# Kernel optimization log

Hardware: AMD Instinct MI355X
Metric: run time of the kernel (lower is better)

Reference implementation:

```python
import jax, jax.numpy as jnp
import numpy as np

DIM = 4096
EPS = 1e-5


def setup_inputs() -> dict:
    key = jax.random.key(0)
    k_x, k_w, k_b, k_g, k_be = jax.random.split(key, 5)
    x = jax.random.normal(k_x, (4, 4096, DIM), dtype=jnp.float32)
    # Linear params (PyTorch default init scale ~ 1/sqrt(dim))
    scale = 1.0 / np.sqrt(DIM)
    W = jax.random.uniform(k_w, (DIM, DIM), dtype=jnp.float32, minval=-scale, maxval=scale)
    b = jax.random.uniform(k_b, (DIM,), dtype=jnp.float32, minval=-scale, maxval=scale)
    # LayerNorm affine params
    gamma = jnp.ones((DIM,), dtype=jnp.float32)
    beta = jnp.zeros((DIM,), dtype=jnp.float32)
    return {"x": x, "W": W, "b": b, "gamma": gamma, "beta": beta}


def reference(x, W, b, gamma, beta) -> jnp.ndarray:
    # LayerNorm over last dim (eps=1e-5, matching nn.LayerNorm default)
    mean = jnp.mean(x, axis=-1, keepdims=True)
    var = jnp.mean(jnp.square(x - mean), axis=-1, keepdims=True)
    h = (x - mean) * jax.lax.rsqrt(var + EPS) * gamma + beta
    # Linear: y = h @ W^T + b  (torch Linear stores W as [out, in])
    y = jnp.einsum("bsd,ed->bse", h, W) + b
    # ReLU
    return jnp.maximum(y, 0.0)
```

## Files before the change

kernel.cpp:

```cpp
#include <hip/hip_runtime.h>

#define DIM 4096
#define MROWS 16384
#define EPSV 1e-5f
#define NKT (DIM / 64)

typedef __attribute__((ext_vector_type(8))) short short8;
typedef __attribute__((ext_vector_type(4))) float floatx4;

__device__ __forceinline__ unsigned short f2bf(float f) {
  union { float f; unsigned u; } c; c.f = f;
  unsigned r = c.u + 0x7fffu + ((c.u >> 16) & 1u);
  return (unsigned short)(r >> 16);
}

struct alignas(16) US8 { unsigned short u[8]; };

__global__ __launch_bounds__(256) void ln_kernel(const float* __restrict__ x,
                                                 const float* __restrict__ gamma,
                                                 const float* __restrict__ beta,
                                                 unsigned short* __restrict__ h) {
  const int row  = blockIdx.x * 4 + (threadIdx.x >> 6);
  const int lane = threadIdx.x & 63;
  const float4* xr = (const float4*)(x + (size_t)row * DIM);
  float4 v[16];
  float s = 0.f, s2 = 0.f;
#pragma unroll
  for (int t = 0; t < 8; ++t) {
    const int idx = lane * 2 + t * 128;
    v[2 * t]     = xr[idx];
    v[2 * t + 1] = xr[idx + 1];
#pragma unroll
    for (int j = 0; j < 2; ++j) {
      const float4 q = v[2 * t + j];
      s  += q.x + q.y + q.z + q.w;
      s2 += q.x * q.x + q.y * q.y + q.z * q.z + q.w * q.w;
    }
  }
#pragma unroll
  for (int off = 32; off > 0; off >>= 1) {
    s  += __shfl_xor(s, off);
    s2 += __shfl_xor(s2, off);
  }
  const float mean = s * (1.f / DIM);
  const float var  = s2 * (1.f / DIM) - mean * mean;
  const float rstd = rsqrtf(var + EPSV);
  const float4* g4 = (const float4*)gamma;
  const float4* b4 = (const float4*)beta;
  US8* hr = (US8*)(h + (size_t)row * DIM);
#pragma unroll
  for (int t = 0; t < 8; ++t) {
    const int idx = lane * 2 + t * 128;
    US8 o;
#pragma unroll
    for (int j = 0; j < 2; ++j) {
      const float4 g = g4[idx + j], b = b4[idx + j], q = v[2 * t + j];
      o.u[4 * j + 0] = f2bf((q.x - mean) * rstd * g.x + b.x);
      o.u[4 * j + 1] = f2bf((q.y - mean) * rstd * g.y + b.y);
      o.u[4 * j + 2] = f2bf((q.z - mean) * rstd * g.z + b.z);
      o.u[4 * j + 3] = f2bf((q.w - mean) * rstd * g.w + b.w);
    }
    hr[lane + t * 64] = o;
  }
}

__global__ __launch_bounds__(256) void wconv(const float* __restrict__ W,
                                             unsigned short* __restrict__ Wb) {
  const int i = blockIdx.x * 256 + threadIdx.x;
  const float4 w0 = ((const float4*)W)[2 * i];
  const float4 w1 = ((const float4*)W)[2 * i + 1];
  US8 o;
  o.u[0] = f2bf(w0.x); o.u[1] = f2bf(w0.y); o.u[2] = f2bf(w0.z); o.u[3] = f2bf(w0.w);
  o.u[4] = f2bf(w1.x); o.u[5] = f2bf(w1.y); o.u[6] = f2bf(w1.z); o.u[7] = f2bf(w1.w);
  ((US8*)Wb)[i] = o;
}

template <int MH, int NH>
__device__ __forceinline__ void mma_q(floatx4 acc[8][4], const short8 a[2][4], const short8 b[2][2]) {
  __builtin_amdgcn_s_setprio(1);
#pragma unroll
  for (int ks = 0; ks < 2; ++ks)
#pragma unroll
    for (int mf = 0; mf < 4; ++mf)
#pragma unroll
      for (int nf = 0; nf < 2; ++nf)
        acc[MH * 4 + mf][NH * 2 + nf] = __builtin_amdgcn_mfma_f32_16x16x32_bf16(
            a[ks][mf], b[ks][nf], acc[MH * 4 + mf][NH * 2 + nf], 0, 0, 0);
  __builtin_amdgcn_s_setprio(0);
}

#define BAR()    __builtin_amdgcn_s_barrier()
#define LGKM0()  asm volatile("s_waitcnt lgkmcnt(0)" ::: "memory")
#define VMCNT4() asm volatile("s_waitcnt vmcnt(4)" ::: "memory")
#define VMCNT0() asm volatile("s_waitcnt vmcnt(0)" ::: "memory")

__global__ __launch_bounds__(512, 2) void gemm_bt(const unsigned short* __restrict__ A,
                                                  const unsigned short* __restrict__ B,
                                                  const float* __restrict__ bias,
                                                  float* __restrict__ out) {
  __shared__ short8 As8[4096];
  __shared__ short8 Bs8[4096];
  const int tid  = threadIdx.x;
  const int lane = tid & 63, wave = tid >> 6;
  const int warp_m = wave >> 2, warp_n = wave & 3;
  const int fr = lane & 15;
  const int cg = lane >> 4;

  const int pid = blockIdx.x;
  const int xcd = pid & 7;
  const int s   = pid >> 3;
  const int bm0 = (s >> 1) * 256;
  const int bn0 = (xcd * 2 + (s & 1)) * 256;

  auto stage = [&](const unsigned short* __restrict__ g, short8* lds, int rowbase, int k0, int h) {
#pragma unroll
    for (int i = 0; i < 2; ++i) {
      const int q = i * 512 + wave * 64 + lane;
      const int r = h * 128 + (q >> 3);
      const int c = (q & 7) ^ (r & 7);
      const unsigned short* src = g + (size_t)(rowbase + r) * DIM + k0 + c * 8;
      __builtin_amdgcn_global_load_lds((const __attribute__((address_space(1))) void*)src,
                                       (__attribute__((address_space(3))) void*)(lds + h * 1024 + i * 512 + wave * 64),
                                       16, 0, 0);
    }
  };
  auto ld_a = [&](short8 a[2][4], int buf, int rbase) {
#pragma unroll
    for (int ks = 0; ks < 2; ++ks)
#pragma unroll
      for (int mf = 0; mf < 4; ++mf) {
        const int r = rbase + mf * 16 + fr;
        a[ks][mf] = As8[buf * 2048 + r * 8 + ((ks * 4 + cg) ^ (r & 7))];
      }
  };
  auto ld_b = [&](short8 b[2][2], int buf, int rbase) {
#pragma unroll
    for (int ks = 0; ks < 2; ++ks)
#pragma unroll
      for (int nf = 0; nf < 2; ++nf) {
        const int r = rbase + nf * 16 + fr;
        b[ks][nf] = Bs8[buf * 2048 + r * 8 + ((ks * 4 + cg) ^ (r & 7))];
      }
  };

  floatx4 acc[8][4];
#pragma unroll
  for (int i = 0; i < 8; ++i)
#pragma unroll
    for (int j = 0; j < 4; ++j)
#pragma unroll
      for (int r = 0; r < 4; ++r) acc[i][j][r] = 0.f;

  const int Ra0 = warp_m * 128;
  const int Rb0 = warp_n * 64;

  stage(A, As8, bm0, 0, 0);
  stage(A, As8, bm0, 0, 1);
  stage(B, Bs8, bn0, 0, 0);
  stage(B, Bs8, bn0, 0, 1);
  stage(B, Bs8 + 2048, bn0, 64, 0);
  stage(B, Bs8 + 2048, bn0, 64, 1);
  VMCNT4();
  BAR();

  short8 a[2][4], b0[2][2], b1[2][2];

  for (int it = 0; it < NKT / 2; ++it) {
    const int kO  = it * 128 + 64;
    const int kE2 = (2 * it + 2 < NKT ? 2 * it + 2 : NKT - 1) * 64;
    const int kO2 = (2 * it + 3 < NKT ? 2 * it + 3 : NKT - 1) * 64;

    ld_a(a, 0, Ra0);
    ld_b(b0, 0, Rb0);
    stage(A, As8 + 2048, bm0, kO, 0);
    BAR(); LGKM0();
    mma_q<0, 0>(acc, a, b0);
    BAR();

    ld_b(b1, 0, Rb0 + 32);
    stage(A, As8 + 2048, bm0, kO, 1);
    BAR(); LGKM0();
    mma_q<0, 1>(acc, a, b1);
    BAR();

    ld_a(a, 0, Ra0 + 64);
    stage(B, Bs8, bn0, kE2, 0);
    BAR(); LGKM0();
    mma_q<1, 0>(acc, a, b0);
    BAR();

    stage(B, Bs8, bn0, kE2, 1);
    VMCNT4();
    BAR(); LGKM0();
    mma_q<1, 1>(acc, a, b1);
    BAR();

    ld_a(a, 1, Ra0);
    ld_b(b0, 1, Rb0);
    stage(A, As8, bm0, kE2, 0);
    BAR(); LGKM0();
    mma_q<0, 0>(acc, a, b0);
    BAR();

    ld_b(b1, 1, Rb0 + 32);
    stage(A, As8, bm0, kE2, 1);
    BAR(); LGKM0();
    mma_q<0, 1>(acc, a, b1);
    BAR();

    ld_a(a, 1, Ra0 + 64);
    stage(B, Bs8 + 2048, bn0, kO2, 0);
    BAR(); LGKM0();
    mma_q<1, 0>(acc, a, b0);
    BAR();

    stage(B, Bs8 + 2048, bn0, kO2, 1);
    VMCNT4();
    BAR(); LGKM0();
    mma_q<1, 1>(acc, a, b1);
    BAR();
  }

  VMCNT0();

#pragma unroll
  for (int nh = 0; nh < 2; ++nh)
#pragma unroll
    for (int nf = 0; nf < 2; ++nf) {
      const int col = bn0 + warp_n * 64 + nh * 32 + nf * 16 + fr;
      const float bv = bias[col];
#pragma unroll
      for (int mh = 0; mh < 2; ++mh)
#pragma unroll
        for (int mf = 0; mf < 4; ++mf) {
          const int rbase = bm0 + warp_m * 128 + mh * 64 + mf * 16 + cg * 4;
          const floatx4 v = acc[mh * 4 + mf][nh * 2 + nf];
#pragma unroll
          for (int r = 0; r < 4; ++r)
            out[(size_t)(rbase + r) * DIM + col] = fmaxf(v[r] + bv, 0.f);
        }
    }
}

__global__ __launch_bounds__(256) void fallback_kernel(const float* __restrict__ x,
                                                       const float* __restrict__ W,
                                                       const float* __restrict__ bias,
                                                       const float* __restrict__ gamma,
                                                       const float* __restrict__ beta,
                                                       float* __restrict__ out) {
  __shared__ float h[DIM];
  __shared__ float red[8];
  const int row = blockIdx.x, tid = threadIdx.x;
  const float4* xr = (const float4*)(x + (size_t)row * DIM);
  float s = 0.f, s2 = 0.f;
  float4 v[4];
#pragma unroll
  for (int i = 0; i < 4; ++i) {
    v[i] = xr[tid + i * 256];
    s  += v[i].x + v[i].y + v[i].z + v[i].w;
    s2 += v[i].x * v[i].x + v[i].y * v[i].y + v[i].z * v[i].z + v[i].w * v[i].w;
  }
#pragma unroll
  for (int off = 32; off > 0; off >>= 1) {
    s  += __shfl_down(s, off);
    s2 += __shfl_down(s2, off);
  }
  const int lane = tid & 63, wave = tid >> 6;
  if (lane == 0) { red[wave] = s; red[wave + 4] = s2; }
  __syncthreads();
  s  = red[0] + red[1] + red[2] + red[3];
  s2 = red[4] + red[5] + red[6] + red[7];
  const float mean = s * (1.f / DIM);
  const float var  = s2 * (1.f / DIM) - mean * mean;
  const float rstd = rsqrtf(var + EPSV);
#pragma unroll
  for (int i = 0; i < 4; ++i) {
    const int idx = tid + i * 256;
    const float4 g = ((const float4*)gamma)[idx];
    const float4 b = ((const float4*)beta)[idx];
    float4 o;
    o.x = (v[i].x - mean) * rstd * g.x + b.x;
    o.y = (v[i].y - mean) * rstd * g.y + b.y;
    o.z = (v[i].z - mean) * rstd * g.z + b.z;
    o.w = (v[i].w - mean) * rstd * g.w + b.w;
    ((float4*)h)[idx] = o;
  }
  __syncthreads();
  for (int n = tid; n < DIM; n += 256) {
    const float4* wr = (const float4*)(W + (size_t)n * DIM);
    float acc = 0.f;
    for (int k = 0; k < DIM / 4; ++k) {
      const float4 w = wr[k];
      const float4 hv = ((const float4*)h)[k];
      acc += hv.x * w.x + hv.y * w.y + hv.z * w.z + hv.w * w.w;
    }
    out[(size_t)row * DIM + n] = fmaxf(acc + bias[n], 0.f);
  }
}

extern "C" void kernel_launch(void* const* d_in, const int* in_sizes, int n_in,
                              void* d_out, int out_size, void* d_ws, size_t ws_size,
                              hipStream_t stream) {
  const float* x     = (const float*)d_in[0];
  const float* W     = (const float*)d_in[1];
  const float* b     = (const float*)d_in[2];
  const float* gamma = (const float*)d_in[3];
  const float* beta  = (const float*)d_in[4];
  float* out = (float*)d_out;

  const size_t h_elems = (size_t)MROWS * DIM;
  const size_t w_elems = (size_t)DIM * DIM;
  const size_t need = (h_elems + w_elems) * sizeof(unsigned short);

  if (ws_size >= need) {
    unsigned short* h  = (unsigned short*)d_ws;
    unsigned short* Wb = h + h_elems;
    ln_kernel<<<MROWS / 4, 256, 0, stream>>>(x, gamma, beta, h);
    wconv<<<(int)(w_elems / 8 / 256), 256, 0, stream>>>(W, Wb);
    gemm_bt<<<(MROWS / 256) * (DIM / 256), 512, 0, stream>>>(h, Wb, b, out);
  } else {
    fallback_kernel<<<MROWS, 256, 0, stream>>>(x, W, b, gamma, beta, out);
  }
}
```

Measured before the change: 965.2 us.

## Switch GEMM inner loop to 32x32x16 bf16 MFMA with restructured fragment loads

Replaces the 16x16x32 MFMA tiling with 32x32x16 bf16 MFMA instructions. Each wave now accumulates 4x2 tiles of 32x32 in floatx16 registers, and LDS fragment loads and the epilogue row/column mapping are reworked to match. The pipeline is regrouped: the B-stage step merges two former sub-phases into one barrier section with more MFMAs, and A rows 64-127 are loaded across all four k-slices at once. The aim is fewer MFMA issues and fewer LDS reads per FLOP, plus fewer barriers. In exchange it uses more registers for fragments, which could pressure occupancy at 2 blocks per CU.

```diff
diff --git a/kernel.cpp b/kernel.cpp
--- a/kernel.cpp
+++ b/kernel.cpp
@@ -6,7 +6,7 @@
 #define NKT (DIM / 64)
 
 typedef __attribute__((ext_vector_type(8))) short short8;
-typedef __attribute__((ext_vector_type(4))) float floatx4;
+typedef __attribute__((ext_vector_type(16))) float floatx16;
 
 __device__ __forceinline__ unsigned short f2bf(float f) {
   union { float f; unsigned u; } c; c.f = f;
@@ -75,19 +75,6 @@
   ((US8*)Wb)[i] = o;
 }
 
-template <int MH, int NH>
-__device__ __forceinline__ void mma_q(floatx4 acc[8][4], const short8 a[2][4], const short8 b[2][2]) {
-  __builtin_amdgcn_s_setprio(1);
-#pragma unroll
-  for (int ks = 0; ks < 2; ++ks)
-#pragma unroll
-    for (int mf = 0; mf < 4; ++mf)
-#pragma unroll
-      for (int nf = 0; nf < 2; ++nf)
-        acc[MH * 4 + mf][NH * 2 + nf] = __builtin_amdgcn_mfma_f32_16x16x32_bf16(
-            a[ks][mf], b[ks][nf], acc[MH * 4 + mf][NH * 2 + nf], 0, 0, 0);
-  __builtin_amdgcn_s_setprio(0);
-}
 
 #define BAR()    __builtin_amdgcn_s_barrier()
 #define LGKM0()  asm volatile("s_waitcnt lgkmcnt(0)" ::: "memory")
@@ -103,8 +90,7 @@
   const int tid  = threadIdx.x;
   const int lane = tid & 63, wave = tid >> 6;
   const int warp_m = wave >> 2, warp_n = wave & 3;
-  const int fr = lane & 15;
-  const int cg = lane >> 4;
+  const int l32  = lane & 31, half = lane >> 5;
 
   const int pid = blockIdx.x;
   const int xcd = pid & 7;
@@ -124,35 +110,22 @@
                                        16, 0, 0);
     }
   };
-  auto ld_a = [&](short8 a[2][4], int buf, int rbase) {
-#pragma unroll
-    for (int ks = 0; ks < 2; ++ks)
-#pragma unroll
-      for (int mf = 0; mf < 4; ++mf) {
-        const int r = rbase + mf * 16 + fr;
-        a[ks][mf] = As8[buf * 2048 + r * 8 + ((ks * 4 + cg) ^ (r & 7))];
-      }
+  auto ld_af = [&](int buf, int mt, int ks) -> short8 {
+    const int r = warp_m * 128 + mt * 32 + l32;
+    return As8[buf * 2048 + r * 8 + ((ks * 2 + half) ^ (r & 7))];
   };
-  auto ld_b = [&](short8 b[2][2], int buf, int rbase) {
-#pragma unroll
-    for (int ks = 0; ks < 2; ++ks)
-#pragma unroll
-      for (int nf = 0; nf < 2; ++nf) {
-        const int r = rbase + nf * 16 + fr;
-        b[ks][nf] = Bs8[buf * 2048 + r * 8 + ((ks * 4 + cg) ^ (r & 7))];
-      }
+  auto ld_bf = [&](int buf, int nt, int ks) -> short8 {
+    const int r = warp_n * 64 + nt * 32 + l32;
+    return Bs8[buf * 2048 + r * 8 + ((ks * 2 + half) ^ (r & 7))];
   };
 
-  floatx4 acc[8][4];
-#pragma unroll
-  for (int i = 0; i < 8; ++i)
-#pragma unroll
-    for (int j = 0; j < 4; ++j)
-#pragma unroll
-      for (int r = 0; r < 4; ++r) acc[i][j][r] = 0.f;
-
-  const int Ra0 = warp_m * 128;
-  const int Rb0 = warp_n * 64;
+  floatx16 acc[4][2];
+#pragma unroll
+  for (int i = 0; i < 4; ++i)
+#pragma unroll
+    for (int j = 0; j < 2; ++j)
+#pragma unroll
+      for (int r = 0; r < 16; ++r) acc[i][j][r] = 0.f;
 
   stage(A, As8, bm0, 0, 0);
   stage(A, As8, bm0, 0, 1);
@@ -163,83 +136,167 @@
   VMCNT4();
   BAR();
 
-  short8 a[2][4], b0[2][2], b1[2][2];
+  short8 a01[2][2], b01[2][2], b23[2][2], a23[2][4];
 
   for (int it = 0; it < NKT / 2; ++it) {
     const int kO  = it * 128 + 64;
     const int kE2 = (2 * it + 2 < NKT ? 2 * it + 2 : NKT - 1) * 64;
     const int kO2 = (2 * it + 3 < NKT ? 2 * it + 3 : NKT - 1) * 64;
 
-    ld_a(a, 0, Ra0);
-    ld_b(b0, 0, Rb0);
+#pragma unroll
+    for (int mt = 0; mt < 2; ++mt)
+#pragma unroll
+      for (int ks = 0; ks < 2; ++ks) a01[mt][ks] = ld_af(0, mt, ks);
+#pragma unroll
+    for (int ks = 0; ks < 2; ++ks)
+#pragma unroll
+      for (int nt = 0; nt < 2; ++nt) b01[ks][nt] = ld_bf(0, nt, ks);
     stage(A, As8 + 2048, bm0, kO, 0);
     BAR(); LGKM0();
-    mma_q<0, 0>(acc, a, b0);
-    BAR();
-
-    ld_b(b1, 0, Rb0 + 32);
+    __builtin_amdgcn_s_setprio(1);
+#pragma unroll
+    for (int ks = 0; ks < 2; ++ks)
+#pragma unroll
+      for (int mt = 0; mt < 2; ++mt)
+#pragma unroll
+        for (int nt = 0; nt < 2; ++nt)
+          acc[mt][nt] = __builtin_amdgcn_mfma_f32_32x32x16_bf16(a01[mt][ks], b01[ks][nt], acc[mt][nt], 0, 0, 0);
+    __builtin_amdgcn_s_setprio(0);
+    BAR();
+
+#pragma unroll
+    for (int mt = 0; mt < 2; ++mt)
+#pragma unroll
+      for (int ks = 0; ks < 2; ++ks) a01[mt][ks] = ld_af(0, mt, ks + 2);
+#pragma unroll
+    for (int ks = 0; ks < 2; ++ks)
+#pragma unroll
+      for (int nt = 0; nt < 2; ++nt) b23[ks][nt] = ld_bf(0, nt, ks + 2);
     stage(A, As8 + 2048, bm0, kO, 1);
     BAR(); LGKM0();
-    mma_q<0, 1>(acc, a, b1);
-    BAR();
-
-    ld_a(a, 0, Ra0 + 64);
+    __builtin_amdgcn_s_setprio(1);
+#pragma unroll
+    for (int ks = 0; ks < 2; ++ks)
+#pragma unroll
+      for (int mt = 0; mt < 2; ++mt)
+#pragma unroll
+        for (int nt = 0; nt < 2; ++nt)
+          acc[mt][nt] = __builtin_amdgcn_mfma_f32_32x32x16_bf16(a01[mt][ks], b23[ks][nt], acc[mt][nt], 0, 0, 0);
+    __builtin_amdgcn_s_setprio(0);
+    BAR();
+
+#pragma unroll
+    for (int mt = 0; mt < 2; ++mt)
+#pragma unroll
+      for (int ks = 0; ks < 4; ++ks) a23[mt][ks] = ld_af(0, mt + 2, ks);
     stage(B, Bs8, bn0, kE2, 0);
-    BAR(); LGKM0();
-    mma_q<1, 0>(acc, a, b0);
-    BAR();
-
     stage(B, Bs8, bn0, kE2, 1);
     VMCNT4();
     BAR(); LGKM0();
-    mma_q<1, 1>(acc, a, b1);
-    BAR();
-
-    ld_a(a, 1, Ra0);
-    ld_b(b0, 1, Rb0);
+    __builtin_amdgcn_s_setprio(1);
+#pragma unroll
+    for (int ks = 0; ks < 2; ++ks)
+#pragma unroll
+      for (int mt = 0; mt < 2; ++mt)
+#pragma unroll
+        for (int nt = 0; nt < 2; ++nt)
+          acc[mt + 2][nt] = __builtin_amdgcn_mfma_f32_32x32x16_bf16(a23[mt][ks], b01[ks][nt], acc[mt + 2][nt], 0, 0, 0);
+#pragma unroll
+    for (int ks = 0; ks < 2; ++ks)
+#pragma unroll
+      for (int mt = 0; mt < 2; ++mt)
+#pragma unroll
+        for (int nt = 0; nt < 2; ++nt)
+          acc[mt + 2][nt] = __builtin_amdgcn_mfma_f32_32x32x16_bf16(a23[mt][ks + 2], b23[ks][nt], acc[mt + 2][nt], 0, 0, 0);
+    __builtin_amdgcn_s_setprio(0);
+    BAR();
+
+#pragma unroll
+    for (int mt = 0; mt < 2; ++mt)
+#pragma unroll
+      for (int ks = 0; ks < 2; ++ks) a01[mt][ks] = ld_af(1, mt, ks);
+#pragma unroll
+    for (int ks = 0; ks < 2; ++ks)
+#pragma unroll
+      for (int nt = 0; nt < 2; ++nt) b01[ks][nt] = ld_bf(1, nt, ks);
     stage(A, As8, bm0, kE2, 0);
     BAR(); LGKM0();
-    mma_q<0, 0>(acc, a, b0);
-    BAR();
-
-    ld_b(b1, 1, Rb0 + 32);
+    __builtin_amdgcn_s_setprio(1);
+#pragma unroll
+    for (int ks = 0; ks < 2; ++ks)
+#pragma unroll
+      for (int mt = 0; mt < 2; ++mt)
+#pragma unroll
+        for (int nt = 0; nt < 2; ++nt)
+          acc[mt][nt] = __builtin_amdgcn_mfma_f32_32x32x16_bf16(a01[mt][ks], b01[ks][nt], acc[mt][nt], 0, 0, 0);
+    __builtin_amdgcn_s_setprio(0);
+    BAR();
+
+#pragma unroll
+    for (int mt = 0; mt < 2; ++mt)
+#pragma unroll
+      for (int ks = 0; ks < 2; ++ks) a01[mt][ks] = ld_af(1, mt, ks + 2);
+#pragma unroll
+    for (int ks = 0; ks < 2; ++ks)
+#pragma unroll
+      for (int nt = 0; nt < 2; ++nt) b23[ks][nt] = ld_bf(1, nt, ks + 2);
     stage(A, As8, bm0, kE2, 1);
     BAR(); LGKM0();
-    mma_q<0, 1>(acc, a, b1);
-    BAR();
-
-    ld_a(a, 1, Ra0 + 64);
+    __builtin_amdgcn_s_setprio(1);
+#pragma unroll
+    for (int ks = 0; ks < 2; ++ks)
+#pragma unroll
+      for (int mt = 0; mt < 2; ++mt)
+#pragma unroll
+        for (int nt = 0; nt < 2; ++nt)
+          acc[mt][nt] = __builtin_amdgcn_mfma_f32_32x32x16_bf16(a01[mt][ks], b23[ks][nt], acc[mt][nt], 0, 0, 0);
+    __builtin_amdgcn_s_setprio(0);
+    BAR();
+
+#pragma unroll
+    for (int mt = 0; mt < 2; ++mt)
+#pragma unroll
+      for (int ks = 0; ks < 4; ++ks) a23[mt][ks] = ld_af(1, mt + 2, ks);
     stage(B, Bs8 + 2048, bn0, kO2, 0);
-    BAR(); LGKM0();
-    mma_q<1, 0>(acc, a, b0);
-    BAR();
-
     stage(B, Bs8 + 2048, bn0, kO2, 1);
     VMCNT4();
     BAR(); LGKM0();
-    mma_q<1, 1>(acc, a, b1);
+    __builtin_amdgcn_s_setprio(1);
+#pragma unroll
+    for (int ks = 0; ks < 2; ++ks)
+#pragma unroll
+      for (int mt = 0; mt < 2; ++mt)
+#pragma unroll
+        for (int nt = 0; nt < 2; ++nt)
+          acc[mt + 2][nt] = __builtin_amdgcn_mfma_f32_32x32x16_bf16(a23[mt][ks], b01[ks][nt], acc[mt + 2][nt], 0, 0, 0);
+#pragma unroll
+    for (int ks = 0; ks < 2; ++ks)
+#pragma unroll
+      for (int mt = 0; mt < 2; ++mt)
+#pragma unroll
+        for (int nt = 0; nt < 2; ++nt)
+          acc[mt + 2][nt] = __builtin_amdgcn_mfma_f32_32x32x16_bf16(a23[mt][ks + 2], b23[ks][nt], acc[mt + 2][nt], 0, 0, 0);
+    __builtin_amdgcn_s_setprio(0);
     BAR();
   }
 
   VMCNT0();
 
 #pragma unroll
-  for (int nh = 0; nh < 2; ++nh)
-#pragma unroll
-    for (int nf = 0; nf < 2; ++nf) {
-      const int col = bn0 + warp_n * 64 + nh * 32 + nf * 16 + fr;
-      const float bv = bias[col];
-#pragma unroll
-      for (int mh = 0; mh < 2; ++mh)
-#pragma unroll
-        for (int mf = 0; mf < 4; ++mf) {
-          const int rbase = bm0 + warp_m * 128 + mh * 64 + mf * 16 + cg * 4;
-          const floatx4 v = acc[mh * 4 + mf][nh * 2 + nf];
-#pragma unroll
-          for (int r = 0; r < 4; ++r)
-            out[(size_t)(rbase + r) * DIM + col] = fmaxf(v[r] + bv, 0.f);
-        }
-    }
+  for (int nt = 0; nt < 2; ++nt) {
+    const int col = bn0 + warp_n * 64 + nt * 32 + l32;
+    const float bv = bias[col];
+#pragma unroll
+    for (int mt = 0; mt < 4; ++mt) {
+      const int rbase = bm0 + warp_m * 128 + mt * 32 + 4 * half;
+      const floatx16 v = acc[mt][nt];
+#pragma unroll
+      for (int reg = 0; reg < 16; ++reg) {
+        const int row = rbase + (reg & 3) + 8 * (reg >> 2);
+        out[(size_t)row * DIM + col] = fmaxf(v[reg] + bv, 0.f);
+      }
+    }
+  }
 }
 
 __global__ __launch_bounds__(256) void fallback_kernel(const float* __restrict__ x,
```

Result: slower. 1.066 ms (+10.4%).
